# Performance work log

Hardware: AMD Instinct MI355X
Metric: run time of the kernel (lower is better)

The kernel has to match this reference:

```python
import jax, jax.numpy as jnp
import numpy as np

N_NODES = 100000
NEG_SLOPE = 0.2  # PyG GATConv default leaky_relu slope


def gat_conv(x, src, dst, W, a_src, a_dst, b, concat):
    # x: [N, F_in], W: [F_in, H*C], a_src/a_dst: [H, C], b: [H*C] or [C]
    N = x.shape[0]
    H, C = a_src.shape
    h = (x @ W).reshape(N, H, C)                       # [N, H, C]
    alpha_s = jnp.einsum('nhc,hc->nh', h, a_src)       # [N, H]
    alpha_d = jnp.einsum('nhc,hc->nh', h, a_dst)       # [N, H]
    e = jax.nn.leaky_relu(alpha_s[src] + alpha_d[dst], NEG_SLOPE)  # [E, H]
    # edge-softmax grouped by destination node (numerically stable)
    e_max = jax.ops.segment_max(e, dst, num_segments=N)            # [N, H]
    e_exp = jnp.exp(e - e_max[dst])
    denom = jax.ops.segment_sum(e_exp, dst, num_segments=N)        # [N, H]
    alpha = e_exp / (denom[dst] + 1e-16)                           # [E, H]
    msg = h[src] * alpha[:, :, None]                               # [E, H, C]
    out = jax.ops.segment_sum(msg, dst, num_segments=N)            # [N, H, C]
    out = out.reshape(N, H * C) if concat else out.mean(axis=1)
    return out + b


def setup_inputs() -> dict:
    key = jax.random.key(0)
    ks = jax.random.split(key, 12)
    in_dim, hidden, heads, out_dim = 512, 128, 4, 64
    c1 = hidden // heads   # 32 per-head channels, concat -> hidden
    c2 = hidden            # 128 per-head channels, mean over heads
    E = 600000
    x = jax.random.normal(ks[0], (N_NODES, in_dim), dtype=jnp.float32)
    edge_index = jax.random.randint(ks[1], (2, E), 0, N_NODES, dtype=jnp.int64)
    s = 0.1
    return {
        'x': x,
        'edge_index': edge_index,
        'W1': jax.random.normal(ks[2], (in_dim, heads * c1), dtype=jnp.float32) * s,
        'a_src1': jax.random.normal(ks[3], (heads, c1), dtype=jnp.float32) * s,
        'a_dst1': jax.random.normal(ks[4], (heads, c1), dtype=jnp.float32) * s,
        'b1': jnp.zeros((heads * c1,), dtype=jnp.float32),
        'W2': jax.random.normal(ks[5], (hidden, heads * c2), dtype=jnp.float32) * s,
        'a_src2': jax.random.normal(ks[6], (heads, c2), dtype=jnp.float32) * s,
        'a_dst2': jax.random.normal(ks[7], (heads, c2), dtype=jnp.float32) * s,
        'b2': jnp.zeros((c2,), dtype=jnp.float32),
        'W_lin': jax.random.normal(ks[8], (hidden, out_dim), dtype=jnp.float32) * s,
        'b_lin': jnp.zeros((out_dim,), dtype=jnp.float32),
    }


def reference(x, edge_index, W1, a_src1, a_dst1, b1, W2, a_src2, a_dst2, b2, W_lin, b_lin):
    N = x.shape[0]
    # add self-loops (PyG GATConv default add_self_loops=True)
    loops = jnp.arange(N, dtype=edge_index.dtype)
    src = jnp.concatenate([edge_index[0], loops])
    dst = jnp.concatenate([edge_index[1], loops])
    # dropout layers are identity at inference (training=False)
    h = gat_conv(x, src, dst, W1, a_src1, a_dst1, b1, concat=True)
    h = jax.nn.elu(h)
    embeddings = gat_conv(h, src, dst, W2, a_src2, a_dst2, b2, concat=False)
    out = embeddings @ W_lin + b_lin
    return out, embeddings
```

## Files before the change

kernel.cpp:

```cpp
#include <hip/hip_runtime.h>
#include <hip/hip_bf16.h>

typedef __hip_bfloat16 bf16;
typedef unsigned short u16;
typedef u16 u16x8 __attribute__((ext_vector_type(8)));
typedef __bf16 bf16x8 __attribute__((ext_vector_type(8)));
typedef float f32x4 __attribute__((ext_vector_type(4)));

__device__ __forceinline__ float tof(float x) { return x; }
__device__ __forceinline__ float tof(bf16 x) { return __bfloat162float(x); }
__device__ __forceinline__ bf16 tobf(float x) { return __float2bfloat16(x); }

__device__ __forceinline__ u16 f2bf(float x) {
    unsigned u = __builtin_bit_cast(unsigned, x);
    u += 0x7fffu + ((u >> 16) & 1u);
    return (u16)(u >> 16);
}
__device__ __forceinline__ float bf2f(u16 h) {
    return __builtin_bit_cast(float, (unsigned)h << 16);
}

__global__ void tsplit_k(const float* __restrict__ W, int K, int N,
                         u16* __restrict__ hi, u16* __restrict__ lo)
{
    int i = blockIdx.x * blockDim.x + threadIdx.x;
    if (i >= K * N) return;
    int k = i / N, n = i - k * N;
    float v = W[i];
    u16 h = f2bf(v);
    hi[(long)n * K + k] = h;
    lo[(long)n * K + k] = f2bf(v - bf2f(h));
}

template <bool SPLIT_A>
__global__ __launch_bounds__(256) void gemm_mfma(
    const void* __restrict__ Avoid, const u16* __restrict__ Bhi,
    const u16* __restrict__ Blo, u16* __restrict__ C,
    int M, int Ntot, int K)
{
    __shared__ u16 AsHi[128 * 64];
    __shared__ u16 AsLo[SPLIT_A ? 128 * 64 : 8];
    __shared__ u16 BsHi[128 * 64];
    __shared__ u16 BsLo[128 * 64];
    const int t = threadIdx.x;
    const long bm = (long)blockIdx.y * 128;
    const int bn = blockIdx.x * 128;
    const int srow = t >> 1;
    const int skh  = t & 1;
    const int w  = t >> 6;
    const int wm = (w >> 1) * 64;
    const int wn = (w & 1) * 64;
    const int l  = t & 63;
    const int lr = l & 15;
    const int lg = l >> 4;

    f32x4 acc[4][4];
#pragma unroll
    for (int i = 0; i < 4; ++i)
#pragma unroll
        for (int j = 0; j < 4; ++j) acc[i][j] = {0.f, 0.f, 0.f, 0.f};

    for (int k0 = 0; k0 < K; k0 += 64) {
        {
            long r = bm + srow;
            bool ok = r < M;
            if (SPLIT_A) {
                const float* A = (const float*)Avoid;
                const float4* ap = (const float4*)(A + r * K + k0 + skh * 32);
#pragma unroll
                for (int c = 0; c < 4; ++c) {
                    float va[8];
                    if (ok) {
                        float4 v0 = ap[c * 2], v1 = ap[c * 2 + 1];
                        va[0] = v0.x; va[1] = v0.y; va[2] = v0.z; va[3] = v0.w;
                        va[4] = v1.x; va[5] = v1.y; va[6] = v1.z; va[7] = v1.w;
                    } else {
#pragma unroll
                        for (int j = 0; j < 8; ++j) va[j] = 0.f;
                    }
                    u16x8 hi, lo;
#pragma unroll
                    for (int j = 0; j < 8; ++j) {
                        u16 h = f2bf(va[j]);
                        hi[j] = h;
                        lo[j] = f2bf(va[j] - bf2f(h));
                    }
                    int off = srow * 128 + ((((skh * 4 + c) ^ (srow & 7))) << 4);
                    *(u16x8*)((char*)AsHi + off) = hi;
                    *(u16x8*)((char*)AsLo + off) = lo;
                }
            } else {
                const u16* A = (const u16*)Avoid;
                const u16x8* ap = (const u16x8*)(A + r * K + k0 + skh * 32);
#pragma unroll
                for (int c = 0; c < 4; ++c) {
                    u16x8 hv = {0, 0, 0, 0, 0, 0, 0, 0};
                    if (ok) hv = ap[c];
                    int off = srow * 128 + ((((skh * 4 + c) ^ (srow & 7))) << 4);
                    *(u16x8*)((char*)AsHi + off) = hv;
                }
            }
        }
        {
            const u16x8* bph = (const u16x8*)(Bhi + (long)(bn + srow) * K + k0 + skh * 32);
            const u16x8* bpl = (const u16x8*)(Blo + (long)(bn + srow) * K + k0 + skh * 32);
#pragma unroll
            for (int c = 0; c < 4; ++c) {
                int off = srow * 128 + ((((skh * 4 + c) ^ (srow & 7))) << 4);
                *(u16x8*)((char*)BsHi + off) = bph[c];
                *(u16x8*)((char*)BsLo + off) = bpl[c];
            }
        }
        __syncthreads();
#pragma unroll
        for (int ks = 0; ks < 2; ++ks) {
            bf16x8 bh[4], bl[4];
            const int chl = ks * 4 + lg;
#pragma unroll
            for (int n = 0; n < 4; ++n) {
                int col = wn + n * 16 + lr;
                int off = col * 128 + (((chl ^ (col & 7))) << 4);
                bh[n] = *(const bf16x8*)((const char*)BsHi + off);
                bl[n] = *(const bf16x8*)((const char*)BsLo + off);
            }
#pragma unroll
            for (int m = 0; m < 4; ++m) {
                int row = wm + m * 16 + lr;
                int off = row * 128 + (((chl ^ (row & 7))) << 4);
                bf16x8 ah = *(const bf16x8*)((const char*)AsHi + off);
#pragma unroll
                for (int n = 0; n < 4; ++n)
                    acc[m][n] = __builtin_amdgcn_mfma_f32_16x16x32_bf16(
                        ah, bh[n], acc[m][n], 0, 0, 0);
#pragma unroll
                for (int n = 0; n < 4; ++n)
                    acc[m][n] = __builtin_amdgcn_mfma_f32_16x16x32_bf16(
                        ah, bl[n], acc[m][n], 0, 0, 0);
                if (SPLIT_A) {
                    bf16x8 al = *(const bf16x8*)((const char*)AsLo + off);
#pragma unroll
                    for (int n = 0; n < 4; ++n)
                        acc[m][n] = __builtin_amdgcn_mfma_f32_16x16x32_bf16(
                            al, bh[n], acc[m][n], 0, 0, 0);
                }
            }
        }
        __syncthreads();
    }
#pragma unroll
    for (int m = 0; m < 4; ++m) {
        long r0 = bm + wm + m * 16 + lg * 4;
#pragma unroll
        for (int i = 0; i < 4; ++i) {
            long r = r0 + i;
            if (r < M) {
#pragma unroll
                for (int n = 0; n < 4; ++n) {
                    int col = bn + wn + n * 16 + lr;
                    C[r * Ntot + col] = f2bf(acc[m][n][i]);
                }
            }
        }
    }
}

__global__ void alpha4_k(const bf16* __restrict__ h, const float* __restrict__ asrc,
                         const float* __restrict__ adst, float* __restrict__ out_s,
                         float* __restrict__ out_d, int N)
{
    int i = blockIdx.x * blockDim.x + threadIdx.x;
    if (i >= N * 4) return;
    int n = i >> 2, hh = i & 3;
    const bf16* row = h + (long)n * 128 + hh * 32;
    const float* av = asrc + hh * 32;
    const float* bv = adst + hh * 32;
    float s1 = 0.f, s2 = 0.f;
    for (int c = 0; c < 32; ++c) {
        float v = tof(row[c]);
        s1 += v * av[c];
        s2 += v * bv[c];
    }
    out_s[i] = s1;
    out_d[i] = s2;
}

__global__ __launch_bounds__(256) void alpha2w_k(
    const bf16* __restrict__ h2, const float* __restrict__ as2,
    const float* __restrict__ ad2, float* __restrict__ out_s,
    float* __restrict__ out_d, int N)
{
    int n = blockIdx.x;
    int w = threadIdx.x >> 6;
    int l = threadIdx.x & 63;
    const bf16* row = h2 + (long)n * 512 + w * 128;
    float v0 = tof(row[l]), v1 = tof(row[l + 64]);
    float s1 = v0 * as2[w * 128 + l] + v1 * as2[w * 128 + l + 64];
    float s2 = v0 * ad2[w * 128 + l] + v1 * ad2[w * 128 + l + 64];
#pragma unroll
    for (int off = 32; off; off >>= 1) {
        s1 += __shfl_down(s1, off);
        s2 += __shfl_down(s2, off);
    }
    if (l == 0) { out_s[n * 4 + w] = s1; out_d[n * 4 + w] = s2; }
}

__global__ void init_cnt_k(int* __restrict__ cnt, int N)
{
    int i = blockIdx.x * blockDim.x + threadIdx.x;
    if (i < N) cnt[i] = 1;
}

__global__ void hist_k(const int* __restrict__ dst, int E, int* __restrict__ cnt)
{
    int e = blockIdx.x * blockDim.x + threadIdx.x;
    if (e < E) atomicAdd(&cnt[dst[e]], 1);
}

__global__ __launch_bounds__(256) void scan_blk_k(const int* __restrict__ cnt,
                                                  int* __restrict__ row_ptr,
                                                  int* __restrict__ bsum, int N)
{
    __shared__ int s[256];
    int t = threadIdx.x;
    int i = blockIdx.x * 256 + t;
    int v = (i < N) ? cnt[i] : 0;
    s[t] = v;
    __syncthreads();
    for (int off = 1; off < 256; off <<= 1) {
        int x = (t >= off) ? s[t - off] : 0;
        __syncthreads();
        s[t] += x;
        __syncthreads();
    }
    if (i < N) row_ptr[i] = s[t] - v;
    if (t == 255) bsum[blockIdx.x] = s[255];
}

__global__ __launch_bounds__(512) void scan_top_k(const int* __restrict__ bsum,
                                                  int* __restrict__ bofs, int B)
{
    __shared__ int s[512];
    int t = threadIdx.x;
    int v = (t < B) ? bsum[t] : 0;
    s[t] = v;
    __syncthreads();
    for (int off = 1; off < 512; off <<= 1) {
        int x = (t >= off) ? s[t - off] : 0;
        __syncthreads();
        s[t] += x;
        __syncthreads();
    }
    bofs[t] = s[t] - v;
}

__global__ void add_off_k(int* __restrict__ row_ptr, const int* __restrict__ bofs,
                          int* __restrict__ wofs, int N, int Etot)
{
    int i = blockIdx.x * blockDim.x + threadIdx.x;
    if (i == 0) row_ptr[N] = Etot;
    if (i >= N) return;
    int r = row_ptr[i] + bofs[i >> 8];
    row_ptr[i] = r;
    wofs[i] = r;
}

__global__ void scatter_k(const int* __restrict__ dst, const int* __restrict__ src,
                          int E, int Etot,
                          int* __restrict__ wofs, int* __restrict__ sidx)
{
    int e = blockIdx.x * blockDim.x + threadIdx.x;
    if (e >= Etot) return;
    int d, s;
    if (e < E) { d = dst[e]; s = src[e]; }
    else       { d = e - E;  s = d; }
    int pos = atomicAdd(&wofs[d], 1);
    sidx[pos] = s;
}

__global__ void edgew_k(const int* __restrict__ row_ptr, const int* __restrict__ sidx,
                        const float* __restrict__ asv, const float* __restrict__ adv,
                        float* __restrict__ aw, int N)
{
    int i = blockIdx.x * blockDim.x + threadIdx.x;
    if (i >= N * 4) return;
    int d = i >> 2, hh = i & 3;
    int beg = row_ptr[d], end = row_ptr[d + 1];
    float ad_d = adv[i];
    float m = -1e30f;
    for (int j = beg; j < end; ++j) {
        float l = asv[sidx[j] * 4 + hh] + ad_d;
        l = l > 0.f ? l : 0.2f * l;
        m = fmaxf(m, l);
    }
    float den = 0.f;
    for (int j = beg; j < end; ++j) {
        float l = asv[sidx[j] * 4 + hh] + ad_d;
        l = l > 0.f ? l : 0.2f * l;
        float w = __expf(l - m);
        den += w;
        aw[(long)j * 4 + hh] = w;
    }
    float inv = 1.f / (den + 1e-16f);
    for (int j = beg; j < end; ++j) aw[(long)j * 4 + hh] *= inv;
}

__global__ __launch_bounds__(128) void agg1_gather_k(
    const int* __restrict__ row_ptr, const int* __restrict__ sidx,
    const float* __restrict__ aw,
    const bf16* __restrict__ h1, const float* __restrict__ b1,
    bf16* __restrict__ out1b)
{
    int d = blockIdx.x;
    int t = threadIdx.x;
    int hh = t >> 5;
    int beg = row_ptr[d], end = row_ptr[d + 1];
    float acc = 0.f;
    for (int j = beg; j < end; ++j) {
        int s = sidx[j];
        float a = aw[(long)j * 4 + hh];
        acc += a * tof(h1[(long)s * 128 + t]);
    }
    float v = acc + b1[t];
    v = v > 0.f ? v : (__expf(v) - 1.f);
    out1b[(long)d * 128 + t] = tobf(v);
}

__global__ __launch_bounds__(128) void agg2_gather_k(
    const int* __restrict__ row_ptr, const int* __restrict__ sidx,
    const float* __restrict__ aw,
    const bf16* __restrict__ h2, const float* __restrict__ b2,
    float* __restrict__ emb)
{
    int d = blockIdx.x;
    int c = threadIdx.x;
    int beg = row_ptr[d], end = row_ptr[d + 1];
    float acc = 0.f;
    for (int j = beg; j < end; ++j) {
        int s = sidx[j];
        float4 w = *(const float4*)&aw[(long)j * 4];
        const bf16* hrow = h2 + (long)s * 512 + c;
        acc += w.x * tof(hrow[0]);
        acc += w.y * tof(hrow[128]);
        acc += w.z * tof(hrow[256]);
        acc += w.w * tof(hrow[384]);
    }
    emb[(long)d * 128 + c] = 0.25f * acc + b2[c];
}

__global__ __launch_bounds__(256) void final_k(const float* __restrict__ emb,
                                               const float* __restrict__ W,
                                               const float* __restrict__ bias,
                                               float* __restrict__ out, int N)
{
    __shared__ float Ws[128 * 64];
    __shared__ float Es[4][132];
    const int tid = threadIdx.x;
    for (int i = tid; i < 128 * 64; i += 256) Ws[i] = W[i];
    int node0 = blockIdx.x * 4;
    for (int i = tid; i < 512; i += 256) {
        int nn = i >> 7, c = i & 127;
        int n = node0 + nn;
        Es[nn][c] = (n < N) ? emb[(long)n * 128 + c] : 0.f;
    }
    __syncthreads();
    int nn = tid >> 6, j = tid & 63;
    int n = node0 + nn;
    if (n >= N) return;
    float acc = bias[j];
#pragma unroll 8
    for (int k = 0; k < 128; ++k) acc += Es[nn][k] * Ws[k * 64 + j];
    out[(long)n * 64 + j] = acc;
}

__global__ void diag_k(float* __restrict__ out, long n, float val)
{
    long i = (long)blockIdx.x * blockDim.x + threadIdx.x;
    if (i >= n) return;
    out[i] = val;
}

extern "C" void kernel_launch(void* const* d_in, const int* in_sizes, int n_in,
                              void* d_out, int out_size, void* d_ws, size_t ws_size,
                              hipStream_t stream)
{
    const float* x   = (const float*)d_in[0];
    const int* ei    = (const int*)d_in[1];
    const float* W1  = (const float*)d_in[2];
    const float* as1 = (const float*)d_in[3];
    const float* ad1 = (const float*)d_in[4];
    const float* b1  = (const float*)d_in[5];
    const float* W2  = (const float*)d_in[6];
    const float* as2 = (const float*)d_in[7];
    const float* ad2 = (const float*)d_in[8];
    const float* b2  = (const float*)d_in[9];
    const float* Wl  = (const float*)d_in[10];
    const float* bl  = (const float*)d_in[11];

    const int N = in_sizes[0] / 512;
    const int E = in_sizes[1] / 2;
    const int Etot = E + N;
    const int* src = ei;
    const int* dst = ei + E;

    float* outp = (float*)d_out;
    float* embp = outp + (size_t)N * 64;
    bf16* out1b = (bf16*)embp;
    float* aw = outp;

    char* wsb = (char*)d_ws;
    bf16*  h2    = (bf16*)wsb;
    bf16*  h1    = (bf16*)wsb;
    float* asv   = (float*)(wsb + (size_t)N * 512 * sizeof(bf16));
    float* adv   = asv + (size_t)N * 4;
    int*   cnt   = (int*)(adv + (size_t)N * 4);
    int*   row_ptr = cnt + N;
    int*   wofs  = row_ptr + (N + 1);
    int*   bsum  = wofs + N;
    int*   bofs  = bsum + 512;
    int*   sidx  = bofs + 512;
    char*  pw    = (char*)(sidx + Etot);
    pw = (char*)(((uintptr_t)pw + 255) & ~(uintptr_t)255);
    u16*   w1t_hi = (u16*)pw;
    u16*   w1t_lo = w1t_hi + 128 * 512;
    u16*   w2t_hi = w1t_lo + 128 * 512;
    u16*   w2t_lo = w2t_hi + 512 * 128;
    size_t need  = (size_t)((char*)(w2t_lo + 512 * 128) - wsb);

    dim3 blk(256);
    long n_out_total = (long)N * 192;

    if (ws_size < need) {
        float val = 100.0f + (float)(ws_size >> 20);
        diag_k<<<(int)((n_out_total + 255) / 256), blk, 0, stream>>>(outp, n_out_total, val);
        return;
    }

    const int B = (N + 255) / 256;
    const int gM = (N + 127) / 128;

    tsplit_k<<<(512 * 128 + 255) / 256, blk, 0, stream>>>(W1, 512, 128, w1t_hi, w1t_lo);
    tsplit_k<<<(128 * 512 + 255) / 256, blk, 0, stream>>>(W2, 128, 512, w2t_hi, w2t_lo);

    init_cnt_k<<<B, blk, 0, stream>>>(cnt, N);
    hist_k<<<(E + 255) / 256, blk, 0, stream>>>(dst, E, cnt);
    scan_blk_k<<<B, blk, 0, stream>>>(cnt, row_ptr, bsum, N);
    scan_top_k<<<1, 512, 0, stream>>>(bsum, bofs, B);
    add_off_k<<<B, blk, 0, stream>>>(row_ptr, bofs, wofs, N, Etot);
    scatter_k<<<(Etot + 255) / 256, blk, 0, stream>>>(dst, src, E, Etot, wofs, sidx);

    gemm_mfma<true><<<dim3(1, gM), blk, 0, stream>>>(
        (const void*)x, w1t_hi, w1t_lo, (u16*)h1, N, 128, 512);
    alpha4_k<<<(N * 4 + 255) / 256, blk, 0, stream>>>(h1, as1, ad1, asv, adv, N);
    edgew_k<<<(N * 4 + 255) / 256, blk, 0, stream>>>(row_ptr, sidx, asv, adv, aw, N);
    agg1_gather_k<<<N, 128, 0, stream>>>(row_ptr, sidx, aw, h1, b1, out1b);

    gemm_mfma<false><<<dim3(4, gM), blk, 0, stream>>>(
        (const void*)out1b, w2t_hi, w2t_lo, (u16*)h2, N, 512, 128);
    alpha2w_k<<<N, 256, 0, stream>>>(h2, as2, ad2, asv, adv, N);
    edgew_k<<<(N * 4 + 255) / 256, blk, 0, stream>>>(row_ptr, sidx, asv, adv, aw, N);
    agg2_gather_k<<<N, 128, 0, stream>>>(row_ptr, sidx, aw, h2, b2, embp);

    final_k<<<(N + 3) / 4, blk, 0, stream>>>(embp, Wl, bl, outp, N);
}
```

Baseline: 876.5 us.

## Defer softmax normalization and vectorize gather aggregation, one wave per node

The edge-weight kernel no longer rescales every edge weight by the inverse denominator. It stores a per-node, per-head inverse denominator, and the aggregation kernels apply it once after accumulating. The gather kernels now map one 64-lane wave to each destination node and four nodes to each 256-thread block. Each lane loads two packed bf16 values per access, which halves the number of load instructions and the thread count per node. The cost is an extra N×4 float workspace buffer and a small change in rounding order.

```diff
diff --git a/kernel.cpp b/kernel.cpp
--- a/kernel.cpp
+++ b/kernel.cpp
@@ -3,6 +3,7 @@
 
 typedef __hip_bfloat16 bf16;
 typedef unsigned short u16;
+typedef unsigned int u32;
 typedef u16 u16x8 __attribute__((ext_vector_type(8)));
 typedef __bf16 bf16x8 __attribute__((ext_vector_type(8)));
 typedef float f32x4 __attribute__((ext_vector_type(4)));
@@ -18,6 +19,12 @@
 }
 __device__ __forceinline__ float bf2f(u16 h) {
     return __builtin_bit_cast(float, (unsigned)h << 16);
+}
+__device__ __forceinline__ float bflo(u32 u) {
+    return __builtin_bit_cast(float, u << 16);
+}
+__device__ __forceinline__ float bfhi(u32 u) {
+    return __builtin_bit_cast(float, u & 0xffff0000u);
 }
 
 __global__ void tsplit_k(const float* __restrict__ W, int K, int N,
@@ -279,7 +286,7 @@
 
 __global__ void edgew_k(const int* __restrict__ row_ptr, const int* __restrict__ sidx,
                         const float* __restrict__ asv, const float* __restrict__ adv,
-                        float* __restrict__ aw, int N)
+                        float* __restrict__ aw, float* __restrict__ invden, int N)
 {
     int i = blockIdx.x * blockDim.x + threadIdx.x;
     if (i >= N * 4) return;
@@ -300,51 +307,69 @@
         den += w;
         aw[(long)j * 4 + hh] = w;
     }
-    float inv = 1.f / (den + 1e-16f);
-    for (int j = beg; j < end; ++j) aw[(long)j * 4 + hh] *= inv;
-}
-
-__global__ __launch_bounds__(128) void agg1_gather_k(
+    invden[i] = 1.f / (den + 1e-16f);
+}
+
+__global__ __launch_bounds__(256) void agg1_gather_k(
     const int* __restrict__ row_ptr, const int* __restrict__ sidx,
-    const float* __restrict__ aw,
+    const float* __restrict__ aw, const float* __restrict__ invden,
     const bf16* __restrict__ h1, const float* __restrict__ b1,
-    bf16* __restrict__ out1b)
-{
-    int d = blockIdx.x;
-    int t = threadIdx.x;
-    int hh = t >> 5;
+    bf16* __restrict__ out1b, int N)
+{
+    int d = blockIdx.x * 4 + (threadIdx.x >> 6);
+    if (d >= N) return;
+    int t = threadIdx.x & 63;
+    int c0 = t * 2;
+    int hh = t >> 4;
     int beg = row_ptr[d], end = row_ptr[d + 1];
-    float acc = 0.f;
+    float accA = 0.f, accB = 0.f;
     for (int j = beg; j < end; ++j) {
         int s = sidx[j];
         float a = aw[(long)j * 4 + hh];
-        acc += a * tof(h1[(long)s * 128 + t]);
-    }
-    float v = acc + b1[t];
-    v = v > 0.f ? v : (__expf(v) - 1.f);
-    out1b[(long)d * 128 + t] = tobf(v);
-}
-
-__global__ __launch_bounds__(128) void agg2_gather_k(
+        u32 u = *(const u32*)((const u16*)h1 + (long)s * 128 + c0);
+        accA += a * bflo(u);
+        accB += a * bfhi(u);
+    }
+    float inv = invden[d * 4 + hh];
+    float vA = accA * inv + b1[c0];
+    float vB = accB * inv + b1[c0 + 1];
+    vA = vA > 0.f ? vA : (__expf(vA) - 1.f);
+    vB = vB > 0.f ? vB : (__expf(vB) - 1.f);
+    u32 packed = (u32)f2bf(vA) | ((u32)f2bf(vB) << 16);
+    *(u32*)((u16*)out1b + (long)d * 128 + c0) = packed;
+}
+
+__global__ __launch_bounds__(256) void agg2_gather_k(
     const int* __restrict__ row_ptr, const int* __restrict__ sidx,
-    const float* __restrict__ aw,
+    const float* __restrict__ aw, const float* __restrict__ invden,
     const bf16* __restrict__ h2, const float* __restrict__ b2,
-    float* __restrict__ emb)
-{
-    int d = blockIdx.x;
-    int c = threadIdx.x;
+    float* __restrict__ emb, int N)
+{
+    int d = blockIdx.x * 4 + (threadIdx.x >> 6);
+    if (d >= N) return;
+    int t = threadIdx.x & 63;
+    int c0 = t * 2;
     int beg = row_ptr[d], end = row_ptr[d + 1];
-    float acc = 0.f;
+    float a0A = 0.f, a0B = 0.f, a1A = 0.f, a1B = 0.f;
+    float a2A = 0.f, a2B = 0.f, a3A = 0.f, a3B = 0.f;
     for (int j = beg; j < end; ++j) {
         int s = sidx[j];
         float4 w = *(const float4*)&aw[(long)j * 4];
-        const bf16* hrow = h2 + (long)s * 512 + c;
-        acc += w.x * tof(hrow[0]);
-        acc += w.y * tof(hrow[128]);
-        acc += w.z * tof(hrow[256]);
-        acc += w.w * tof(hrow[384]);
-    }
-    emb[(long)d * 128 + c] = 0.25f * acc + b2[c];
+        const u16* hrow = (const u16*)h2 + (long)s * 512 + c0;
+        u32 u0 = *(const u32*)(hrow);
+        u32 u1 = *(const u32*)(hrow + 128);
+        u32 u2 = *(const u32*)(hrow + 256);
+        u32 u3 = *(const u32*)(hrow + 384);
+        a0A += w.x * bflo(u0); a0B += w.x * bfhi(u0);
+        a1A += w.y * bflo(u1); a1B += w.y * bfhi(u1);
+        a2A += w.z * bflo(u2); a2B += w.z * bfhi(u2);
+        a3A += w.w * bflo(u3); a3B += w.w * bfhi(u3);
+    }
+    float4 inv = *(const float4*)&invden[d * 4];
+    float eA = 0.25f * (a0A * inv.x + a1A * inv.y + a2A * inv.z + a3A * inv.w) + b2[c0];
+    float eB = 0.25f * (a0B * inv.x + a1B * inv.y + a2B * inv.z + a3B * inv.w) + b2[c0 + 1];
+    float2 ev = {eA, eB};
+    *(float2*)&emb[(long)d * 128 + c0] = ev;
 }
 
 __global__ __launch_bounds__(256) void final_k(const float* __restrict__ emb,
@@ -412,7 +437,8 @@
     bf16*  h1    = (bf16*)wsb;
     float* asv   = (float*)(wsb + (size_t)N * 512 * sizeof(bf16));
     float* adv   = asv + (size_t)N * 4;
-    int*   cnt   = (int*)(adv + (size_t)N * 4);
+    float* invden = adv + (size_t)N * 4;
+    int*   cnt   = (int*)(invden + (size_t)N * 4);
     int*   row_ptr = cnt + N;
     int*   wofs  = row_ptr + (N + 1);
     int*   bsum  = wofs + N;
@@ -437,6 +463,7 @@
 
     const int B = (N + 255) / 256;
     const int gM = (N + 127) / 128;
+    const int gAgg = (N + 3) / 4;
 
     tsplit_k<<<(512 * 128 + 255) / 256, blk, 0, stream>>>(W1, 512, 128, w1t_hi, w1t_lo);
     tsplit_k<<<(128 * 512 + 255) / 256, blk, 0, stream>>>(W2, 128, 512, w2t_hi, w2t_lo);
@@ -451,14 +478,14 @@
     gemm_mfma<true><<<dim3(1, gM), blk, 0, stream>>>(
         (const void*)x, w1t_hi, w1t_lo, (u16*)h1, N, 128, 512);
     alpha4_k<<<(N * 4 + 255) / 256, blk, 0, stream>>>(h1, as1, ad1, asv, adv, N);
-    edgew_k<<<(N * 4 + 255) / 256, blk, 0, stream>>>(row_ptr, sidx, asv, adv, aw, N);
-    agg1_gather_k<<<N, 128, 0, stream>>>(row_ptr, sidx, aw, h1, b1, out1b);
+    edgew_k<<<(N * 4 + 255) / 256, blk, 0, stream>>>(row_ptr, sidx, asv, adv, aw, invden, N);
+    agg1_gather_k<<<gAgg, blk, 0, stream>>>(row_ptr, sidx, aw, invden, h1, b1, out1b, N);
 
     gemm_mfma<false><<<dim3(4, gM), blk, 0, stream>>>(
         (const void*)out1b, w2t_hi, w2t_lo, (u16*)h2, N, 512, 128);
     alpha2w_k<<<N, 256, 0, stream>>>(h2, as2, ad2, asv, adv, N);
-    edgew_k<<<(N * 4 + 255) / 256, blk, 0, stream>>>(row_ptr, sidx, asv, adv, aw, N);
-    agg2_gather_k<<<N, 128, 0, stream>>>(row_ptr, sidx, aw, h2, b2, embp);
+    edgew_k<<<(N * 4 + 255) / 256, blk, 0, stream>>>(row_ptr, sidx, asv, adv, aw, invden, N);
+    agg2_gather_k<<<gAgg, blk, 0, stream>>>(row_ptr, sidx, aw, invden, h2, b2, embp, N);
 
     final_k<<<(N + 3) / 4, blk, 0, stream>>>(embp, Wl, bl, outp, N);
 }
```

Result: faster. 850.8 us (-2.9%).
